# Optimization experiments

Measured on AMD Instinct MI355X. Metric: run time of the kernel, lower is better.

## Reference

```python
import jax, jax.numpy as jnp
import numpy as np

B, T, D, H, O = 1024, 2048, 13, 128, 2


def setup_inputs() -> dict:
    key = jax.random.key(0)
    k1, k2, k3, k4 = jax.random.split(key, 4)
    xs = jax.random.normal(k1, (B, T, D), dtype=jnp.float32)
    # nn.Linear(in, out, bias=False) weights: [out, in]
    W_in = jax.random.normal(k2, (H, D), dtype=jnp.float32) / np.sqrt(D).astype(np.float32)
    W_h = jax.random.normal(k3, (H, H), dtype=jnp.float32) / np.sqrt(H).astype(np.float32)
    W_out = jax.random.normal(k4, (O, H), dtype=jnp.float32) / np.sqrt(H).astype(np.float32)
    return {"xs": xs, "W_in": W_in, "W_h": W_h, "W_out": W_out}


def reference(xs, W_in, W_h, W_out):
    # Vanilla hardtanh RNN, h0 = 0 (first step y = hardtanh(in_h(x)) == hardtanh(in_h(x) + W_h @ 0)).
    # Precompute all input projections in one big GEMM: [B, T, H]
    pre = jnp.einsum('btd,hd->bth', xs, W_in)

    def step(h, xh_t):  # h: [B, H], xh_t: [B, H]
        h = jnp.clip(xh_t + h @ W_h.T, -1.0, 1.0)  # F.hardtanh
        return h, None

    h0 = jnp.zeros((xs.shape[0], W_in.shape[0]), dtype=xs.dtype)
    hT, _ = jax.lax.scan(step, h0, jnp.swapaxes(pre, 0, 1))  # scan over time
    # Only the final hidden state per sequence is projected to the output.
    return hT @ W_out.T  # [B, O]
```

## Files before the change

kernel.cpp:

```cpp
#include <hip/hip_runtime.h>
#include <stdint.h>


#define RNN_B 1024
#define RNN_T 2048
#define RNN_D 13
#define RNN_H 128
#define RNN_O 2

#define NB 16
#define NWAVE 4
#define NTHR (NWAVE * 64)
#define MTW 2
#define NKT 5
#define HPAD 136

using f32x4 = __attribute__((ext_vector_type(4))) float;
using v8s   = __attribute__((ext_vector_type(8))) short;

__device__ __forceinline__ short f2bf(float f) {
    union { float f; uint32_t u; } c; c.f = f;
    uint32_t u = c.u + 0x7fffu + ((c.u >> 16) & 1u);
    return (short)(u >> 16);
}
__device__ __forceinline__ float bf2f(short s) {
    union { uint32_t u; float f; } c; c.u = ((uint32_t)(uint16_t)s) << 16;
    return c.f;
}

__global__ __launch_bounds__(NTHR, 1) void rnn_mfma_kernel(
    const float* __restrict__ xs,
    const float* __restrict__ W_in,
    const float* __restrict__ W_h,
    const float* __restrict__ W_out,
    float* __restrict__ out)
{
    __shared__ short hbf_hi[2][NB][HPAD];
    __shared__ short hbf_lo[2][NB][HPAD];

    const int tid  = threadIdx.x;
    const int lane = tid & 63;
    const int wid  = tid >> 6;
    const int n    = lane & 15;
    const int g    = lane >> 4;
    const int b0   = blockIdx.x * NB;

    v8s wa_hi[MTW][NKT], wa_lo[MTW][NKT];
    #pragma unroll
    for (int mi = 0; mi < MTW; ++mi) {
        const int row = 16 * (wid * MTW + mi) + n;
        #pragma unroll
        for (int kt = 0; kt < NKT; ++kt) {
            v8s h8, l8;
            #pragma unroll
            for (int j = 0; j < 4; ++j) {
                float w1, w2;
                if (kt < 4) {
                    w1 = W_h[row * RNN_H + 32 * kt + 4 * g + j];
                    w2 = W_h[row * RNN_H + 32 * kt + 16 + 4 * g + j];
                } else {
                    const int kx = 4 * g + j;
                    w1 = (kx < RNN_D) ? W_in[row * RNN_D + kx] : 0.0f;
                    w2 = 0.0f;
                }
                const short h1 = f2bf(w1);
                const short l1 = f2bf(w1 - bf2f(h1));
                const short h2 = f2bf(w2);
                const short l2 = f2bf(w2 - bf2f(h2));
                h8[j] = h1; h8[4 + j] = h2;
                l8[j] = l1; l8[4 + j] = l2;
            }
            wa_hi[mi][kt] = h8;
            wa_lo[mi][kt] = l8;
        }
    }

    {
        short* z0 = &hbf_hi[0][0][0];
        short* z1 = &hbf_lo[0][0][0];
        for (int idx = tid; idx < NB * HPAD; idx += NTHR) { z0[idx] = 0; z1[idx] = 0; }
    }

    float xv[4];
    {
        const float* xr = xs + ((size_t)(b0 + n) * RNN_T + 0) * RNN_D;
        #pragma unroll
        for (int j = 0; j < 4; ++j) { const int d = 4 * g + j; xv[j] = xr[d > 12 ? 12 : d]; }
    }
    __syncthreads();

    for (int t = 0; t < RNN_T; ++t) {
        const int cur = t & 1, nxt = cur ^ 1;

        v8s xb_hi, xb_lo;
        #pragma unroll
        for (int j = 0; j < 4; ++j) {
            const int d = 4 * g + j;
            const float v = (d < RNN_D) ? xv[j] : 0.0f;
            const short h1 = f2bf(v);
            const short l1 = f2bf(v - bf2f(h1));
            xb_hi[j] = h1; xb_hi[4 + j] = 0;
            xb_lo[j] = l1; xb_lo[4 + j] = 0;
        }

        if (t + 1 < RNN_T) {
            const float* xr = xs + ((size_t)(b0 + n) * RNN_T + (t + 1)) * RNN_D;
            #pragma unroll
            for (int j = 0; j < 4; ++j) { const int d = 4 * g + j; xv[j] = xr[d > 12 ? 12 : d]; }
        }

        v8s bh[4], bl[4];
        #pragma unroll
        for (int kt = 0; kt < 4; ++kt) {
            const short* p = &hbf_hi[cur][n][32 * kt + 4 * g];
            const int2 r1 = *(const int2*)p;
            const int2 r2 = *(const int2*)(p + 16);
            union { int4 i; v8s s; } u; u.i = make_int4(r1.x, r1.y, r2.x, r2.y);
            bh[kt] = u.s;
            const short* q = &hbf_lo[cur][n][32 * kt + 4 * g];
            const int2 s1 = *(const int2*)q;
            const int2 s2 = *(const int2*)(q + 16);
            union { int4 i; v8s s; } v; v.i = make_int4(s1.x, s1.y, s2.x, s2.y);
            bl[kt] = v.s;
        }

        #pragma unroll
        for (int mi = 0; mi < MTW; ++mi) {
            f32x4 a1 = {0.f, 0.f, 0.f, 0.f};
            f32x4 a2 = {0.f, 0.f, 0.f, 0.f};
            f32x4 a3 = {0.f, 0.f, 0.f, 0.f};
            #pragma unroll
            for (int kt = 0; kt < 4; ++kt) {
                a1 = __builtin_amdgcn_mfma_f32_16x16x32_bf16(wa_hi[mi][kt], bh[kt], a1, 0, 0, 0);
                a2 = __builtin_amdgcn_mfma_f32_16x16x32_bf16(wa_hi[mi][kt], bl[kt], a2, 0, 0, 0);
                a3 = __builtin_amdgcn_mfma_f32_16x16x32_bf16(wa_lo[mi][kt], bh[kt], a3, 0, 0, 0);
            }
            a1 = __builtin_amdgcn_mfma_f32_16x16x32_bf16(wa_hi[mi][4], xb_hi, a1, 0, 0, 0);
            a2 = __builtin_amdgcn_mfma_f32_16x16x32_bf16(wa_hi[mi][4], xb_lo, a2, 0, 0, 0);
            a3 = __builtin_amdgcn_mfma_f32_16x16x32_bf16(wa_lo[mi][4], xb_hi, a3, 0, 0, 0);

            short hs[4], ls[4];
            #pragma unroll
            for (int r = 0; r < 4; ++r) {
                float vv = a1[r] + a2[r] + a3[r];
                vv = fminf(fmaxf(vv, -1.0f), 1.0f);
                const short hh = f2bf(vv);
                hs[r] = hh;
                ls[r] = f2bf(vv - bf2f(hh));
            }
            const int krow = 16 * (wid * MTW + mi) + 4 * g;
            int2 ph, pl;
            ph.x = (int)(((uint32_t)(uint16_t)hs[1] << 16) | (uint16_t)hs[0]);
            ph.y = (int)(((uint32_t)(uint16_t)hs[3] << 16) | (uint16_t)hs[2]);
            pl.x = (int)(((uint32_t)(uint16_t)ls[1] << 16) | (uint16_t)ls[0]);
            pl.y = (int)(((uint32_t)(uint16_t)ls[3] << 16) | (uint16_t)ls[2]);
            *(int2*)&hbf_hi[nxt][n][krow] = ph;
            *(int2*)&hbf_lo[nxt][n][krow] = pl;
        }
        __syncthreads();
    }

    if (wid == 0 && lane < NB * RNN_O) {
        const int nn = lane & 15;
        const int o  = lane >> 4;
        float acc = 0.0f;
        for (int i = 0; i < RNN_H; ++i) {
            const float hv = bf2f(hbf_hi[0][nn][i]) + bf2f(hbf_lo[0][nn][i]);
            acc = fmaf(W_out[o * RNN_H + i], hv, acc);
        }
        out[(size_t)(b0 + nn) * RNN_O + o] = acc;
    }
}

extern "C" void kernel_launch(void* const* d_in, const int* in_sizes, int n_in,
                              void* d_out, int out_size, void* d_ws, size_t ws_size,
                              hipStream_t stream) {
    const float* xs    = (const float*)d_in[0];
    const float* W_in  = (const float*)d_in[1];
    const float* W_h   = (const float*)d_in[2];
    const float* W_out = (const float*)d_in[3];
    float* out = (float*)d_out;

    rnn_mfma_kernel<<<RNN_B / NB, NTHR, 0, stream>>>(xs, W_in, W_h, W_out, out);
}
```

Before: 1.255 ms.

## Split hidden rows across eight waves and permute LDS hidden-state layout

Doubles the waves per block from four to eight so each wave owns one 16-row tile of the hidden dimension instead of two. This halves the per-wave serial MFMA chain in each recurrent step. The hidden state in LDS is stored in a permuted order, so each lane reads its B operand with a single 16-byte load instead of two 8-byte loads. The time loop is manually unrolled by two with separate x prefetch registers. In exchange, the per-step __syncthreads now spans eight waves and the final output projection needs index remapping.

```diff
diff --git a/kernel.cpp b/kernel.cpp
--- a/kernel.cpp
+++ b/kernel.cpp
@@ -9,11 +9,10 @@
 #define RNN_O 2
 
 #define NB 16
-#define NWAVE 4
+#define NWAVE 8
 #define NTHR (NWAVE * 64)
-#define MTW 2
 #define NKT 5
-#define HPAD 136
+#define ROWS 136
 
 using f32x4 = __attribute__((ext_vector_type(4))) float;
 using v8s   = __attribute__((ext_vector_type(8))) short;
@@ -28,15 +27,77 @@
     return c.f;
 }
 
-__global__ __launch_bounds__(NTHR, 1) void rnn_mfma_kernel(
+__device__ __forceinline__ void rnn_step(
+    int cur, int nxt, float* xc, int tnext,
+    const float* __restrict__ xrow,
+    const v8s* whi, const v8s* wlo,
+    short (*Hhi)[NB][ROWS], short (*Hlo)[NB][ROWS],
+    int n, int g, int wid)
+{
+    v8s xh, xl;
+    #pragma unroll
+    for (int j = 0; j < 4; ++j) {
+        const int d = 4 * g + j;
+        const float v = (d < RNN_D) ? xc[j] : 0.0f;
+        const short h1 = f2bf(v);
+        xh[j] = h1;                 xh[4 + j] = 0;
+        xl[j] = f2bf(v - bf2f(h1)); xl[4 + j] = 0;
+    }
+    if (tnext < RNN_T) {
+        const float* xp = xrow + (size_t)tnext * RNN_D;
+        #pragma unroll
+        for (int j = 0; j < 4; ++j) { const int d = 4 * g + j; xc[j] = xp[d > 12 ? 12 : d]; }
+    }
+
+    v8s bh[4], bl[4];
+    #pragma unroll
+    for (int kt = 0; kt < 4; ++kt) {
+        bh[kt] = *(const v8s*)&Hhi[cur][n][kt * 32 + g * 8];
+        bl[kt] = *(const v8s*)&Hlo[cur][n][kt * 32 + g * 8];
+    }
+
+    f32x4 a1 = {0.f, 0.f, 0.f, 0.f};
+    f32x4 a2 = {0.f, 0.f, 0.f, 0.f};
+    f32x4 a3 = {0.f, 0.f, 0.f, 0.f};
+    #pragma unroll
+    for (int kt = 0; kt < 4; ++kt) {
+        a1 = __builtin_amdgcn_mfma_f32_16x16x32_bf16(whi[kt], bh[kt], a1, 0, 0, 0);
+        a2 = __builtin_amdgcn_mfma_f32_16x16x32_bf16(whi[kt], bl[kt], a2, 0, 0, 0);
+        a3 = __builtin_amdgcn_mfma_f32_16x16x32_bf16(wlo[kt], bh[kt], a3, 0, 0, 0);
+    }
+    a1 = __builtin_amdgcn_mfma_f32_16x16x32_bf16(whi[4], xh, a1, 0, 0, 0);
+    a2 = __builtin_amdgcn_mfma_f32_16x16x32_bf16(whi[4], xl, a2, 0, 0, 0);
+    a3 = __builtin_amdgcn_mfma_f32_16x16x32_bf16(wlo[4], xh, a3, 0, 0, 0);
+
+    short hs[4], ls[4];
+    #pragma unroll
+    for (int r = 0; r < 4; ++r) {
+        float v = a1[r] + a2[r] + a3[r];
+        v = fminf(fmaxf(v, -1.0f), 1.0f);
+        const short hh = f2bf(v);
+        hs[r] = hh;
+        ls[r] = f2bf(v - bf2f(hh));
+    }
+    int2 ph, pl;
+    ph.x = (int)(((uint32_t)(uint16_t)hs[1] << 16) | (uint16_t)hs[0]);
+    ph.y = (int)(((uint32_t)(uint16_t)hs[3] << 16) | (uint16_t)hs[2]);
+    pl.x = (int)(((uint32_t)(uint16_t)ls[1] << 16) | (uint16_t)ls[0]);
+    pl.y = (int)(((uint32_t)(uint16_t)ls[3] << 16) | (uint16_t)ls[2]);
+    const int wp = (wid >> 1) * 32 + g * 8 + (wid & 1) * 4;
+    *(int2*)&Hhi[nxt][n][wp] = ph;
+    *(int2*)&Hlo[nxt][n][wp] = pl;
+    __syncthreads();
+}
+
+__global__ __launch_bounds__(NTHR, 2) void rnn_mfma8_kernel(
     const float* __restrict__ xs,
     const float* __restrict__ W_in,
     const float* __restrict__ W_h,
     const float* __restrict__ W_out,
     float* __restrict__ out)
 {
-    __shared__ short hbf_hi[2][NB][HPAD];
-    __shared__ short hbf_lo[2][NB][HPAD];
+    __shared__ short Hhi[2][NB][ROWS];
+    __shared__ short Hlo[2][NB][ROWS];
 
     const int tid  = threadIdx.x;
     const int lane = tid & 63;
@@ -45,10 +106,9 @@
     const int g    = lane >> 4;
     const int b0   = blockIdx.x * NB;
 
-    v8s wa_hi[MTW][NKT], wa_lo[MTW][NKT];
-    #pragma unroll
-    for (int mi = 0; mi < MTW; ++mi) {
-        const int row = 16 * (wid * MTW + mi) + n;
+    v8s whi[NKT], wlo[NKT];
+    {
+        const int row = 16 * wid + n;
         #pragma unroll
         for (int kt = 0; kt < NKT; ++kt) {
             v8s h8, l8;
@@ -64,100 +124,34 @@
                     w2 = 0.0f;
                 }
                 const short h1 = f2bf(w1);
-                const short l1 = f2bf(w1 - bf2f(h1));
                 const short h2 = f2bf(w2);
-                const short l2 = f2bf(w2 - bf2f(h2));
                 h8[j] = h1; h8[4 + j] = h2;
-                l8[j] = l1; l8[4 + j] = l2;
+                l8[j] = f2bf(w1 - bf2f(h1));
+                l8[4 + j] = f2bf(w2 - bf2f(h2));
             }
-            wa_hi[mi][kt] = h8;
-            wa_lo[mi][kt] = l8;
+            whi[kt] = h8;
+            wlo[kt] = l8;
         }
     }
 
-    {
-        short* z0 = &hbf_hi[0][0][0];
-        short* z1 = &hbf_lo[0][0][0];
-        for (int idx = tid; idx < NB * HPAD; idx += NTHR) { z0[idx] = 0; z1[idx] = 0; }
+    for (int idx = tid; idx < NB * ROWS; idx += NTHR) {
+        (&Hhi[0][0][0])[idx] = 0;
+        (&Hlo[0][0][0])[idx] = 0;
     }
 
-    float xv[4];
-    {
-        const float* xr = xs + ((size_t)(b0 + n) * RNN_T + 0) * RNN_D;
-        #pragma unroll
-        for (int j = 0; j < 4; ++j) { const int d = 4 * g + j; xv[j] = xr[d > 12 ? 12 : d]; }
+    const float* xrow = xs + (size_t)(b0 + n) * RNN_T * RNN_D;
+    float xa[4], xb[4];
+    #pragma unroll
+    for (int j = 0; j < 4; ++j) {
+        const int d = 4 * g + j;
+        xa[j] = xrow[d > 12 ? 12 : d];
+        xb[j] = xrow[RNN_D + (d > 12 ? 12 : d)];
     }
     __syncthreads();
 
-    for (int t = 0; t < RNN_T; ++t) {
-        const int cur = t & 1, nxt = cur ^ 1;
-
-        v8s xb_hi, xb_lo;
-        #pragma unroll
-        for (int j = 0; j < 4; ++j) {
-            const int d = 4 * g + j;
-            const float v = (d < RNN_D) ? xv[j] : 0.0f;
-            const short h1 = f2bf(v);
-            const short l1 = f2bf(v - bf2f(h1));
-            xb_hi[j] = h1; xb_hi[4 + j] = 0;
-            xb_lo[j] = l1; xb_lo[4 + j] = 0;
-        }
-
-        if (t + 1 < RNN_T) {
-            const float* xr = xs + ((size_t)(b0 + n) * RNN_T + (t + 1)) * RNN_D;
-            #pragma unroll
-            for (int j = 0; j < 4; ++j) { const int d = 4 * g + j; xv[j] = xr[d > 12 ? 12 : d]; }
-        }
-
-        v8s bh[4], bl[4];
-        #pragma unroll
-        for (int kt = 0; kt < 4; ++kt) {
-            const short* p = &hbf_hi[cur][n][32 * kt + 4 * g];
-            const int2 r1 = *(const int2*)p;
-            const int2 r2 = *(const int2*)(p + 16);
-            union { int4 i; v8s s; } u; u.i = make_int4(r1.x, r1.y, r2.x, r2.y);
-            bh[kt] = u.s;
-            const short* q = &hbf_lo[cur][n][32 * kt + 4 * g];
-            const int2 s1 = *(const int2*)q;
-            const int2 s2 = *(const int2*)(q + 16);
-            union { int4 i; v8s s; } v; v.i = make_int4(s1.x, s1.y, s2.x, s2.y);
-            bl[kt] = v.s;
-        }
-
-        #pragma unroll
-        for (int mi = 0; mi < MTW; ++mi) {
-            f32x4 a1 = {0.f, 0.f, 0.f, 0.f};
-            f32x4 a2 = {0.f, 0.f, 0.f, 0.f};
-            f32x4 a3 = {0.f, 0.f, 0.f, 0.f};
-            #pragma unroll
-            for (int kt = 0; kt < 4; ++kt) {
-                a1 = __builtin_amdgcn_mfma_f32_16x16x32_bf16(wa_hi[mi][kt], bh[kt], a1, 0, 0, 0);
-                a2 = __builtin_amdgcn_mfma_f32_16x16x32_bf16(wa_hi[mi][kt], bl[kt], a2, 0, 0, 0);
-                a3 = __builtin_amdgcn_mfma_f32_16x16x32_bf16(wa_lo[mi][kt], bh[kt], a3, 0, 0, 0);
-            }
-            a1 = __builtin_amdgcn_mfma_f32_16x16x32_bf16(wa_hi[mi][4], xb_hi, a1, 0, 0, 0);
-            a2 = __builtin_amdgcn_mfma_f32_16x16x32_bf16(wa_hi[mi][4], xb_lo, a2, 0, 0, 0);
-            a3 = __builtin_amdgcn_mfma_f32_16x16x32_bf16(wa_lo[mi][4], xb_hi, a3, 0, 0, 0);
-
-            short hs[4], ls[4];
-            #pragma unroll
-            for (int r = 0; r < 4; ++r) {
-                float vv = a1[r] + a2[r] + a3[r];
-                vv = fminf(fmaxf(vv, -1.0f), 1.0f);
-                const short hh = f2bf(vv);
-                hs[r] = hh;
-                ls[r] = f2bf(vv - bf2f(hh));
-            }
-            const int krow = 16 * (wid * MTW + mi) + 4 * g;
-            int2 ph, pl;
-            ph.x = (int)(((uint32_t)(uint16_t)hs[1] << 16) | (uint16_t)hs[0]);
-            ph.y = (int)(((uint32_t)(uint16_t)hs[3] << 16) | (uint16_t)hs[2]);
-            pl.x = (int)(((uint32_t)(uint16_t)ls[1] << 16) | (uint16_t)ls[0]);
-            pl.y = (int)(((uint32_t)(uint16_t)ls[3] << 16) | (uint16_t)ls[2]);
-            *(int2*)&hbf_hi[nxt][n][krow] = ph;
-            *(int2*)&hbf_lo[nxt][n][krow] = pl;
-        }
-        __syncthreads();
+    for (int t = 0; t < RNN_T; t += 2) {
+        rnn_step(0, 1, xa, t + 2, xrow, whi, wlo, Hhi, Hlo, n, g, wid);
+        rnn_step(1, 0, xb, t + 3, xrow, whi, wlo, Hhi, Hlo, n, g, wid);
     }
 
     if (wid == 0 && lane < NB * RNN_O) {
@@ -165,7 +159,9 @@
         const int o  = lane >> 4;
         float acc = 0.0f;
         for (int i = 0; i < RNN_H; ++i) {
-            const float hv = bf2f(hbf_hi[0][nn][i]) + bf2f(hbf_lo[0][nn][i]);
+            const int kt = i >> 5, rem = i & 31, half = rem >> 4, r4 = rem & 15;
+            const int pos = kt * 32 + (r4 >> 2) * 8 + half * 4 + (r4 & 3);
+            const float hv = bf2f(Hhi[0][nn][pos]) + bf2f(Hlo[0][nn][pos]);
             acc = fmaf(W_out[o * RNN_H + i], hv, acc);
         }
         out[(size_t)(b0 + nn) * RNN_O + o] = acc;
@@ -181,5 +177,5 @@
     const float* W_out = (const float*)d_in[3];
     float* out = (float*)d_out;
 
-    rnn_mfma_kernel<<<RNN_B / NB, NTHR, 0, stream>>>(xs, W_in, W_h, W_out, out);
+    rnn_mfma8_kernel<<<RNN_B / NB, NTHR, 0, stream>>>(xs, W_in, W_h, W_out, out);
 }
```

Measured after the change: 2.290 ms. 1.82x slower.
